# Optimization experiments

Hardware: AMD Instinct MI355X
Metric: run time of the kernel (lower is better)

## Reference

```python
import jax, jax.numpy as jnp
import numpy as np
from jax import lax

# Module config (from init_kwargs)
PADDING = (1, 1)
DILATION = (1, 1)
GROUPS = 1
# stride param is initialized to ones(2); effective integer stride = floor(stride) = (1, 1).
# Output shape depends on this value, so it must be static under jit.
INT_STRIDE = (1, 1)


def setup_inputs() -> dict:
    key = jax.random.key(0)
    k1, k2 = jax.random.split(key)
    B, Cin, H, W = 32, 128, 64, 64
    Cout, kH, kW = 256, 3, 3
    x = jax.random.normal(k1, (B, Cin, H, W), dtype=jnp.float32)
    # reset_parameters: uniform(-stdv, stdv), stdv = 1/sqrt(Cin*kH*kW)
    stdv = 1.0 / np.sqrt(Cin * kH * kW)
    weight = jax.random.uniform(k2, (Cout, Cin // GROUPS, kH, kW), dtype=jnp.float32,
                                minval=-stdv, maxval=stdv)
    stride = jnp.ones((2,), dtype=jnp.float32)
    return {"x": x, "weight": weight, "stride": stride}


def reference(x, weight, stride):
    # Integer strides = floor(stride); with stride initialized to ones this is (1, 1).
    # (Static under jit; floor has zero derivative a.e., so stride only affects
    #  sampling locations, exactly as in the CUDA im2col forward.)
    out = lax.conv_general_dilated(
        x, weight,
        window_strides=INT_STRIDE,
        padding=[(PADDING[0], PADDING[0]), (PADDING[1], PADDING[1])],
        rhs_dilation=DILATION,
        dimension_numbers=("NCHW", "OIHW", "NCHW"),
        feature_group_count=GROUPS,
    )
    return out
```

## Files before the change

### kernel.cpp

```cpp
#include <hip/hip_runtime.h>

typedef __attribute__((ext_vector_type(8))) short short8;
typedef __attribute__((ext_vector_type(4))) float f32x4;

#define XP_ELEMS (32u * 66u * 66u * 128u)
#define WT_ELEMS (256u * 1152u)
#define WS_NEED  ((size_t)(XP_ELEMS + WT_ELEMS) * 2u)

typedef const __attribute__((address_space(1))) void* gp1_t;
typedef __attribute__((address_space(3))) void* lp3_t;

__device__ __forceinline__ void gload16(const void* g, void* l) {
  __builtin_amdgcn_global_load_lds((gp1_t)g, (lp3_t)l, 16, 0, 0);
}

__device__ __forceinline__ short f2bf(float f) {
  unsigned u = __float_as_uint(f);
  u = (u + 0x7FFFu + ((u >> 16) & 1u)) >> 16;
  return (short)u;
}

__global__ __launch_bounds__(256) void prepass_x(const float* __restrict__ x,
                                                 short* __restrict__ xp) {
  __shared__ short lds[64 * 128];
  const int y = blockIdx.x;
  const int b = blockIdx.y;
  const int t = threadIdx.x;

  const float* src = x + (long)b * 128 * 4096 + y * 64;
#pragma unroll
  for (int i = 0; i < 8; ++i) {
    int f4 = t + i * 256;
    int cin = f4 >> 4, px4 = f4 & 15;
    float4 v = *(const float4*)(src + (long)cin * 4096 + px4 * 4);
    float vv[4] = {v.x, v.y, v.z, v.w};
#pragma unroll
    for (int j = 0; j < 4; ++j) {
      int px = px4 * 4 + j;
      int g = (cin >> 3) ^ ((px ^ (px >> 2)) & 15);
      lds[px * 128 + (g << 3) + (cin & 7)] = f2bf(vv[j]);
    }
  }
  __syncthreads();
  short* dst = xp + ((long)(b * 66 + y + 1) * 66 + 1) * 128;
#pragma unroll
  for (int i = 0; i < 4; ++i) {
    int f8 = t + i * 256;
    int px = f8 >> 4, c8 = f8 & 15;
    int g = c8 ^ ((px ^ (px >> 2)) & 15);
    short8 v = *(const short8*)&lds[px * 128 + (g << 3)];
    *(short8*)(dst + (long)px * 128 + c8 * 8) = v;
  }
  short8 z = (short8)0;
  short* rowbase = xp + (long)(b * 66 + y + 1) * 66 * 128;
  if (t < 32) {
    int px = (t < 16) ? 0 : 65;
    int c8 = t & 15;
    *(short8*)(rowbase + (long)px * 128 + c8 * 8) = z;
  }
  if (y == 0) {
    short* r0 = xp + (long)(b * 66) * 66 * 128;
    for (int idx = t; idx < 66 * 16; idx += 256) *(short8*)(r0 + idx * 8) = z;
  }
  if (y == 63) {
    short* r65 = xp + ((long)(b * 66) + 65) * 66 * 128;
    for (int idx = t; idx < 66 * 16; idx += 256) *(short8*)(r65 + idx * 8) = z;
  }
}

__global__ __launch_bounds__(256) void prepass_w(const float* __restrict__ w,
                                                 short* __restrict__ wt) {
  int o    = blockIdx.x * 256 + threadIdx.x;
  int cout = o / 1152;
  int r    = o % 1152;
  int kh   = r / 384;
  int kw   = (r / 128) % 3;
  int cin  = r & 127;
  wt[o] = f2bf(w[((cout * 128 + cin) * 3 + kh) * 3 + kw]);
}

__global__ __launch_bounds__(256) void conv_gemm(const short* __restrict__ xp,
                                                 const short* __restrict__ wt,
                                                 float* __restrict__ out) {
  __shared__ short Alds[2 * 128 * 32];
  __shared__ short Blds[2 * 128 * 32];
  const int tid   = threadIdx.x;
  const int w     = tid >> 6;
  const int l     = tid & 63;
  const int l15   = l & 15;
  const int q     = l >> 4;
  const int ntile = blockIdx.x;
  const int m0    = blockIdx.y << 7;

  const int srow = (w << 4) + (l >> 2);
  const int sch8 = (((l & 3) ^ ((srow >> 1) & 3)) * 8);

  const long aoff0 = (long)(m0 + srow) * 1152 + sch8;
  const long aoff1 = aoff0 + (long)64 * 1152;

  long boff[2];
#pragma unroll
  for (int c = 0; c < 2; ++c) {
    int ng = (ntile << 7) + (c << 6) + srow;
    int b = ng >> 12, yx = ng & 4095;
    int y = yx >> 6, xx = yx & 63;
    boff[c] = ((long)(b * 66 + y) * 66 + xx) * 128 + sch8;
  }

  short* Adst0 = &Alds[(w << 4) * 32];
  short* Adst1 = Adst0 + 64 * 32;
  short* Bdst0 = &Blds[(w << 4) * 32];
  short* Bdst1 = Bdst0 + 64 * 32;

  f32x4 acc[4][4];
#pragma unroll
  for (int i = 0; i < 4; ++i)
#pragma unroll
    for (int j = 0; j < 4; ++j) acc[i][j] = (f32x4)0.f;

  const int wm = (w >> 1) << 6;
  const int wn = (w & 1) << 6;

#pragma unroll
  for (int khkw = 0; khkw < 9; ++khkw) {
    const int kh = khkw / 3, kw = khkw % 3;
    const long sB = (long)(kh * 66 + kw) * 128;
    const int kkb = khkw << 7;
#pragma unroll
    for (int s = 0; s < 2; ++s) {
#pragma unroll
      for (int c = 0; c < 2; ++c) {
        const int cin0 = (s << 6) + (c << 5);
        const int kk0  = kkb + cin0;
        const int co   = c * 4096;
        gload16(wt + aoff0 + kk0, Adst0 + co);
        gload16(wt + aoff1 + kk0, Adst1 + co);
        gload16(xp + boff[0] + sB + cin0, Bdst0 + co);
        gload16(xp + boff[1] + sB + cin0, Bdst1 + co);
      }
      __syncthreads();
#pragma unroll
      for (int c = 0; c < 2; ++c) {
        const int co = c * 4096;
        short8 af[4], bf[4];
#pragma unroll
        for (int i = 0; i < 4; ++i) {
          int rA = wm + (i << 4) + l15;
          af[i] = *(const short8*)&Alds[co + rA * 32 + ((q ^ ((rA >> 1) & 3)) << 3)];
        }
#pragma unroll
        for (int j = 0; j < 4; ++j) {
          int rB = wn + (j << 4) + l15;
          bf[j] = *(const short8*)&Blds[co + rB * 32 + ((q ^ ((rB >> 1) & 3)) << 3)];
        }
#pragma unroll
        for (int i = 0; i < 4; ++i)
#pragma unroll
          for (int j = 0; j < 4; ++j)
            acc[i][j] = __builtin_amdgcn_mfma_f32_16x16x32_bf16(af[i], bf[j],
                                                                acc[i][j], 0, 0, 0);
      }
      __syncthreads();
    }
  }

  const int ngb = (ntile << 7) + wn;
  const int b   = ngb >> 12;
  const int yxb = ngb & 4095;
  float* outb = out + (long)b * (256 * 4096) + yxb + l15;
#pragma unroll
  for (int i = 0; i < 4; ++i) {
#pragma unroll
    for (int r = 0; r < 4; ++r) {
      const int cout = m0 + wm + (i << 4) + q * 4 + r;
      float* orow = outb + (long)cout * 4096;
#pragma unroll
      for (int j = 0; j < 4; ++j) orow[j * 16] = acc[i][j][r];
    }
  }
}

__global__ __launch_bounds__(256) void naive_conv(const float* __restrict__ x,
                                                  const float* __restrict__ wgt,
                                                  float* __restrict__ out) {
  long o = (long)blockIdx.x * 256 + threadIdx.x;
  int xx = (int)(o & 63);
  int y  = (int)((o >> 6) & 63);
  int co = (int)((o >> 12) & 255);
  int b  = (int)(o >> 20);
  float s = 0.f;
  for (int ci = 0; ci < 128; ++ci) {
    for (int kh = 0; kh < 3; ++kh) {
      int iy = y + kh - 1;
      if (iy < 0 || iy > 63) continue;
      for (int kw = 0; kw < 3; ++kw) {
        int ix = xx + kw - 1;
        if (ix < 0 || ix > 63) continue;
        s += x[((long)(b * 128 + ci) * 64 + iy) * 64 + ix] *
             wgt[((co * 128 + ci) * 3 + kh) * 3 + kw];
      }
    }
  }
  out[o] = s;
}

extern "C" void kernel_launch(void* const* d_in, const int* in_sizes, int n_in,
                              void* d_out, int out_size, void* d_ws, size_t ws_size,
                              hipStream_t stream) {
  (void)in_sizes; (void)n_in;
  const float* x   = (const float*)d_in[0];
  const float* wgt = (const float*)d_in[1];
  float* out = (float*)d_out;
  if (ws_size >= WS_NEED) {
    short* xp = (short*)d_ws;
    short* wt = xp + XP_ELEMS;
    prepass_x<<<dim3(64, 32), dim3(256), 0, stream>>>(x, xp);
    prepass_w<<<dim3(WT_ELEMS / 256), dim3(256), 0, stream>>>(wgt, wt);
    conv_gemm<<<dim3(1024, 2), dim3(256), 0, stream>>>(xp, wt, out);
  } else {
    naive_conv<<<dim3(out_size / 256), dim3(256), 0, stream>>>(x, wgt, out);
  }
}
```

Measured before the change: 264.2 us.

## Enlarge GEMM tile to 256x256 with a 4-stage async LDS pipeline

The implicit-GEMM conv kernel now computes a full 256-cout by 256-pixel tile per 512-thread block, so each block covers all output channels and the input tile is read once instead of twice. A 4-deep ring of LDS buffers is filled with global_load_lds three stages ahead, and explicit vmcnt waits replace the two full barriers per k-step that the old version used. MFMA sections are bracketed with raised wave priority. Each wave now holds 32 accumulators, which raises register pressure, and the grid drops to 512 blocks, which may affect occupancy and load balance across CUs.

Result: faster. 258.3 us (-2.2%).

```diff
diff --git a/kernel.cpp b/kernel.cpp
--- a/kernel.cpp
+++ b/kernel.cpp
@@ -79,103 +79,115 @@
   wt[o] = f2bf(w[((cout * 128 + cin) * 3 + kh) * 3 + kw]);
 }
 
-__global__ __launch_bounds__(256) void conv_gemm(const short* __restrict__ xp,
-                                                 const short* __restrict__ wt,
-                                                 float* __restrict__ out) {
-  __shared__ short Alds[2 * 128 * 32];
-  __shared__ short Blds[2 * 128 * 32];
-  const int tid   = threadIdx.x;
-  const int w     = tid >> 6;
-  const int l     = tid & 63;
-  const int l15   = l & 15;
-  const int q     = l >> 4;
+__global__ __launch_bounds__(512, 2) void conv_gemm(const short* __restrict__ xp,
+                                                    const short* __restrict__ wt,
+                                                    float* __restrict__ out) {
+  __shared__ alignas(16) short Al[4][256 * 32];
+  __shared__ alignas(16) short Bl[4][256 * 32];
+  const int tid = threadIdx.x;
+  const int w   = tid >> 6;
+  const int l   = tid & 63;
+  const int l15 = l & 15;
+  const int q   = l >> 4;
+  const int wm2 = w >> 2;
+  const int wn4 = w & 3;
   const int ntile = blockIdx.x;
-  const int m0    = blockIdx.y << 7;
-
-  const int srow = (w << 4) + (l >> 2);
-  const int sch8 = (((l & 3) ^ ((srow >> 1) & 3)) * 8);
-
-  const long aoff0 = (long)(m0 + srow) * 1152 + sch8;
-  const long aoff1 = aoff0 + (long)64 * 1152;
-
-  long boff[2];
-#pragma unroll
-  for (int c = 0; c < 2; ++c) {
-    int ng = (ntile << 7) + (c << 6) + srow;
-    int b = ng >> 12, yx = ng & 4095;
-    int y = yx >> 6, xx = yx & 63;
-    boff[c] = ((long)(b * 66 + y) * 66 + xx) * 128 + sch8;
-  }
-
-  short* Adst0 = &Alds[(w << 4) * 32];
-  short* Adst1 = Adst0 + 64 * 32;
-  short* Bdst0 = &Blds[(w << 4) * 32];
-  short* Bdst1 = Bdst0 + 64 * 32;
-
-  f32x4 acc[4][4];
-#pragma unroll
-  for (int i = 0; i < 4; ++i)
-#pragma unroll
-    for (int j = 0; j < 4; ++j) acc[i][j] = (f32x4)0.f;
-
-  const int wm = (w >> 1) << 6;
-  const int wn = (w & 1) << 6;
-
-#pragma unroll
-  for (int khkw = 0; khkw < 9; ++khkw) {
-    const int kh = khkw / 3, kw = khkw % 3;
-    const long sB = (long)(kh * 66 + kw) * 128;
-    const int kkb = khkw << 7;
-#pragma unroll
-    for (int s = 0; s < 2; ++s) {
-#pragma unroll
-      for (int c = 0; c < 2; ++c) {
-        const int cin0 = (s << 6) + (c << 5);
-        const int kk0  = kkb + cin0;
-        const int co   = c * 4096;
-        gload16(wt + aoff0 + kk0, Adst0 + co);
-        gload16(wt + aoff1 + kk0, Adst1 + co);
-        gload16(xp + boff[0] + sB + cin0, Bdst0 + co);
-        gload16(xp + boff[1] + sB + cin0, Bdst1 + co);
-      }
-      __syncthreads();
-#pragma unroll
-      for (int c = 0; c < 2; ++c) {
-        const int co = c * 4096;
-        short8 af[4], bf[4];
-#pragma unroll
-        for (int i = 0; i < 4; ++i) {
-          int rA = wm + (i << 4) + l15;
-          af[i] = *(const short8*)&Alds[co + rA * 32 + ((q ^ ((rA >> 1) & 3)) << 3)];
-        }
-#pragma unroll
-        for (int j = 0; j < 4; ++j) {
-          int rB = wn + (j << 4) + l15;
-          bf[j] = *(const short8*)&Blds[co + rB * 32 + ((q ^ ((rB >> 1) & 3)) << 3)];
-        }
-#pragma unroll
-        for (int i = 0; i < 4; ++i)
-#pragma unroll
-          for (int j = 0; j < 4; ++j)
-            acc[i][j] = __builtin_amdgcn_mfma_f32_16x16x32_bf16(af[i], bf[j],
-                                                                acc[i][j], 0, 0, 0);
-      }
-      __syncthreads();
-    }
-  }
-
-  const int ngb = (ntile << 7) + wn;
-  const int b   = ngb >> 12;
-  const int yxb = ngb & 4095;
-  float* outb = out + (long)b * (256 * 4096) + yxb + l15;
-#pragma unroll
-  for (int i = 0; i < 4; ++i) {
+
+  const int r0  = tid >> 2;
+  const int r1  = r0 + 128;
+  const int p0  = tid & 3;
+  const int cs0 = p0 ^ ((r0 >> 1) & 3);
+  const int cs1 = p0 ^ ((r1 >> 1) & 3);
+  const long aoff0 = (long)r0 * 1152 + (cs0 << 3);
+  const long aoff1 = (long)r1 * 1152 + (cs1 << 3);
+
+  long boff0, boff1;
+  {
+    int n0 = (ntile << 8) + r0;
+    int bb = n0 >> 12, yx = n0 & 4095, y = yx >> 6, xx = yx & 63;
+    boff0 = ((long)(bb * 66 + y) * 66 + xx) * 128 + (cs0 << 3);
+    int n1 = n0 + 128;
+    bb = n1 >> 12; yx = n1 & 4095; y = yx >> 6; xx = yx & 63;
+    boff1 = ((long)(bb * 66 + y) * 66 + xx) * 128 + (cs1 << 3);
+  }
+  const int ldst0 = tid * 8;
+  const int ldst1 = (512 + tid) * 8;
+
+  int aRd[8], bRd[4];
+#pragma unroll
+  for (int mi = 0; mi < 8; ++mi) {
+    int r = (wm2 << 7) + (mi << 4) + l15;
+    aRd[mi] = r * 32 + ((q ^ ((r >> 1) & 3)) << 3);
+  }
+#pragma unroll
+  for (int nj = 0; nj < 4; ++nj) {
+    int r = (wn4 << 6) + (nj << 4) + l15;
+    bRd[nj] = r * 32 + ((q ^ ((r >> 1) & 3)) << 3);
+  }
+
+  f32x4 acc[8][4];
+#pragma unroll
+  for (int mi = 0; mi < 8; ++mi)
+#pragma unroll
+    for (int nj = 0; nj < 4; ++nj) acc[mi][nj] = (f32x4)0.f;
+
+  auto STAGE = [&](int kss, int bufS) {
+    const int kq = kss >> 2;
+    const int kh = kq / 3, kw2 = kq % 3;
+    const long sBs = (long)(kh * 66 + kw2) * 128 + ((kss & 3) << 5);
+    const long ka  = (long)kss << 5;
+    gload16(wt + aoff0 + ka, &Al[bufS][ldst0]);
+    gload16(wt + aoff1 + ka, &Al[bufS][ldst1]);
+    gload16(xp + boff0 + sBs, &Bl[bufS][ldst0]);
+    gload16(xp + boff1 + sBs, &Bl[bufS][ldst1]);
+  };
+
+  STAGE(0, 0); STAGE(1, 1); STAGE(2, 2);
+  asm volatile("s_waitcnt vmcnt(8)" ::: "memory");
+  __builtin_amdgcn_s_barrier();
+  __builtin_amdgcn_sched_barrier(0);
+
+#pragma unroll
+  for (int ks = 0; ks < 36; ++ks) {
+    if (ks + 3 < 36) STAGE(ks + 3, (ks + 3) & 3);
+
+    const short* Ab = &Al[ks & 3][0];
+    const short* Bb = &Bl[ks & 3][0];
+    short8 af[8], bf[4];
+#pragma unroll
+    for (int mi = 0; mi < 8; ++mi) af[mi] = *(const short8*)&Ab[aRd[mi]];
+#pragma unroll
+    for (int nj = 0; nj < 4; ++nj) bf[nj] = *(const short8*)&Bb[bRd[nj]];
+
+    __builtin_amdgcn_s_setprio(1);
+#pragma unroll
+    for (int mi = 0; mi < 8; ++mi)
+#pragma unroll
+      for (int nj = 0; nj < 4; ++nj)
+        acc[mi][nj] = __builtin_amdgcn_mfma_f32_16x16x32_bf16(af[mi], bf[nj],
+                                                              acc[mi][nj], 0, 0, 0);
+    __builtin_amdgcn_s_setprio(0);
+
+    if (ks + 1 < 36) {
+      if (ks + 3 < 36)      asm volatile("s_waitcnt vmcnt(8)" ::: "memory");
+      else if (ks + 2 < 36) asm volatile("s_waitcnt vmcnt(4)" ::: "memory");
+      else                  asm volatile("s_waitcnt vmcnt(0)" ::: "memory");
+      __builtin_amdgcn_s_barrier();
+      __builtin_amdgcn_sched_barrier(0);
+    }
+  }
+
+  const int bimg = ntile >> 4;
+  const int yx0  = ((ntile & 15) << 8) + (wn4 << 6) + l15;
+  float* outb = out + (long)bimg * (256 * 4096) + yx0;
+#pragma unroll
+  for (int mi = 0; mi < 8; ++mi) {
 #pragma unroll
     for (int r = 0; r < 4; ++r) {
-      const int cout = m0 + wm + (i << 4) + q * 4 + r;
+      const int cout = (wm2 << 7) + (mi << 4) + (q << 2) + r;
       float* orow = outb + (long)cout * 4096;
 #pragma unroll
-      for (int j = 0; j < 4; ++j) orow[j * 16] = acc[i][j][r];
+      for (int nj = 0; nj < 4; ++nj) orow[nj << 4] = acc[mi][nj][r];
     }
   }
 }
@@ -216,7 +228,7 @@
     short* wt = xp + XP_ELEMS;
     prepass_x<<<dim3(64, 32), dim3(256), 0, stream>>>(x, xp);
     prepass_w<<<dim3(WT_ELEMS / 256), dim3(256), 0, stream>>>(wgt, wt);
-    conv_gemm<<<dim3(1024, 2), dim3(256), 0, stream>>>(xp, wt, out);
+    conv_gemm<<<dim3(512), dim3(512), 0, stream>>>(xp, wt, out);
   } else {
     naive_conv<<<dim3(out_size / 256), dim3(256), 0, stream>>>(x, wgt, out);
   }
```

## Triple-buffer conv GEMM K-loop with async LDS prefetch and one barrier per step

Applied to the files above, without the earlier changes.

Replaces the synchronous two-barrier-per-chunk K loop with a 3-slot ring buffer. Global-to-LDS loads for step k+2 are issued before computing step k, and each step waits only on vmcnt plus a single barrier. It also precomputes LDS read offsets, raises MFMA wave priority with s_setprio, and adds a launch-bounds occupancy hint of 3. The cost is 50% more LDS per block and a reliance on hand-counted vmcnt waits being correct for the buffered loads.

Measured after the change: 277.6 us. +5.1%, slower.

```diff
diff --git a/kernel.cpp b/kernel.cpp
--- a/kernel.cpp
+++ b/kernel.cpp
@@ -79,11 +79,11 @@
   wt[o] = f2bf(w[((cout * 128 + cin) * 3 + kh) * 3 + kw]);
 }
 
-__global__ __launch_bounds__(256) void conv_gemm(const short* __restrict__ xp,
-                                                 const short* __restrict__ wt,
-                                                 float* __restrict__ out) {
-  __shared__ short Alds[2 * 128 * 32];
-  __shared__ short Blds[2 * 128 * 32];
+__global__ __launch_bounds__(256, 3) void conv_gemm(const short* __restrict__ xp,
+                                                    const short* __restrict__ wt,
+                                                    float* __restrict__ out) {
+  __shared__ alignas(16) short Alds[3 * 128 * 32];
+  __shared__ alignas(16) short Blds[3 * 128 * 32];
   const int tid   = threadIdx.x;
   const int w     = tid >> 6;
   const int l     = tid & 63;
@@ -92,77 +92,92 @@
   const int ntile = blockIdx.x;
   const int m0    = blockIdx.y << 7;
 
-  const int srow = (w << 4) + (l >> 2);
-  const int sch8 = (((l & 3) ^ ((srow >> 1) & 3)) * 8);
-
-  const long aoff0 = (long)(m0 + srow) * 1152 + sch8;
+  const int r  = tid >> 2;
+  const int p  = tid & 3;
+  const int cs = p ^ ((r >> 1) & 3);
+  const long aoff0 = (long)(m0 + r) * 1152 + (cs << 3);
   const long aoff1 = aoff0 + (long)64 * 1152;
-
-  long boff[2];
-#pragma unroll
-  for (int c = 0; c < 2; ++c) {
-    int ng = (ntile << 7) + (c << 6) + srow;
-    int b = ng >> 12, yx = ng & 4095;
-    int y = yx >> 6, xx = yx & 63;
-    boff[c] = ((long)(b * 66 + y) * 66 + xx) * 128 + sch8;
-  }
-
-  short* Adst0 = &Alds[(w << 4) * 32];
-  short* Adst1 = Adst0 + 64 * 32;
-  short* Bdst0 = &Blds[(w << 4) * 32];
-  short* Bdst1 = Bdst0 + 64 * 32;
-
-  f32x4 acc[4][4];
-#pragma unroll
-  for (int i = 0; i < 4; ++i)
-#pragma unroll
-    for (int j = 0; j < 4; ++j) acc[i][j] = (f32x4)0.f;
+  long boff0, boff1;
+  {
+    int n0 = (ntile << 7) + r;
+    int bb = n0 >> 12, yy = (n0 >> 6) & 63, xx = n0 & 63;
+    boff0 = ((long)(bb * 66 + yy) * 66 + xx) * 128 + (cs << 3);
+    int n1 = n0 + 64;
+    bb = n1 >> 12; yy = (n1 >> 6) & 63; xx = n1 & 63;
+    boff1 = ((long)(bb * 66 + yy) * 66 + xx) * 128 + (cs << 3);
+  }
+  const int ldst0 = r * 32 + p * 8;
+  const int ldst1 = ldst0 + 2048;
 
   const int wm = (w >> 1) << 6;
   const int wn = (w & 1) << 6;
-
-#pragma unroll
-  for (int khkw = 0; khkw < 9; ++khkw) {
-    const int kh = khkw / 3, kw = khkw % 3;
-    const long sB = (long)(kh * 66 + kw) * 128;
-    const int kkb = khkw << 7;
-#pragma unroll
-    for (int s = 0; s < 2; ++s) {
-#pragma unroll
-      for (int c = 0; c < 2; ++c) {
-        const int cin0 = (s << 6) + (c << 5);
-        const int kk0  = kkb + cin0;
-        const int co   = c * 4096;
-        gload16(wt + aoff0 + kk0, Adst0 + co);
-        gload16(wt + aoff1 + kk0, Adst1 + co);
-        gload16(xp + boff[0] + sB + cin0, Bdst0 + co);
-        gload16(xp + boff[1] + sB + cin0, Bdst1 + co);
-      }
-      __syncthreads();
-#pragma unroll
-      for (int c = 0; c < 2; ++c) {
-        const int co = c * 4096;
-        short8 af[4], bf[4];
-#pragma unroll
-        for (int i = 0; i < 4; ++i) {
-          int rA = wm + (i << 4) + l15;
-          af[i] = *(const short8*)&Alds[co + rA * 32 + ((q ^ ((rA >> 1) & 3)) << 3)];
-        }
-#pragma unroll
-        for (int j = 0; j < 4; ++j) {
-          int rB = wn + (j << 4) + l15;
-          bf[j] = *(const short8*)&Blds[co + rB * 32 + ((q ^ ((rB >> 1) & 3)) << 3)];
-        }
-#pragma unroll
-        for (int i = 0; i < 4; ++i)
-#pragma unroll
-          for (int j = 0; j < 4; ++j)
-            acc[i][j] = __builtin_amdgcn_mfma_f32_16x16x32_bf16(af[i], bf[j],
-                                                                acc[i][j], 0, 0, 0);
-      }
-      __syncthreads();
-    }
-  }
+  int aRd[4], bRd[4];
+#pragma unroll
+  for (int i = 0; i < 4; ++i) {
+    int rA = wm + (i << 4) + l15;
+    aRd[i] = rA * 32 + ((q ^ ((rA >> 1) & 3)) << 3);
+    int rB = wn + (i << 4) + l15;
+    bRd[i] = rB * 32 + ((q ^ ((rB >> 1) & 3)) << 3);
+  }
+
+  f32x4 acc[4][4];
+#pragma unroll
+  for (int i = 0; i < 4; ++i)
+#pragma unroll
+    for (int j = 0; j < 4; ++j) acc[i][j] = (f32x4)0.f;
+
+  auto STAGE = [&](int slot, int ks) {
+    const int kq  = ks >> 2;
+    const int kh  = kq / 3, kw2 = kq - kh * 3;
+    const int sB  = (kh * 66 + kw2) * 128 + ((ks & 3) << 5);
+    const int ka  = ks << 5;
+    short* Ad = &Alds[slot * 4096];
+    short* Bd = &Blds[slot * 4096];
+    gload16(wt + aoff0 + ka, Ad + ldst0);
+    gload16(wt + aoff1 + ka, Ad + ldst1);
+    gload16(xp + boff0 + sB, Bd + ldst0);
+    gload16(xp + boff1 + sB, Bd + ldst1);
+  };
+
+  auto COMPUTE = [&](int slot) {
+    const short* Ab = &Alds[slot * 4096];
+    const short* Bb = &Blds[slot * 4096];
+    short8 af[4], bf[4];
+#pragma unroll
+    for (int i = 0; i < 4; ++i) af[i] = *(const short8*)&Ab[aRd[i]];
+#pragma unroll
+    for (int j = 0; j < 4; ++j) bf[j] = *(const short8*)&Bb[bRd[j]];
+    __builtin_amdgcn_s_setprio(1);
+#pragma unroll
+    for (int i = 0; i < 4; ++i)
+#pragma unroll
+      for (int j = 0; j < 4; ++j)
+        acc[i][j] = __builtin_amdgcn_mfma_f32_16x16x32_bf16(af[i], bf[j],
+                                                            acc[i][j], 0, 0, 0);
+    __builtin_amdgcn_s_setprio(0);
+  };
+
+#define BAR()   __builtin_amdgcn_s_barrier()
+#define VMC(n)  asm volatile("s_waitcnt vmcnt(" #n ")" ::: "memory")
+
+  STAGE(0, 0);
+  STAGE(1, 1);
+  VMC(4);
+  BAR();
+
+  int s_cur = 0, s_nxt = 1, s_stg = 2;
+#pragma unroll 1
+  for (int ks = 0; ks < 34; ++ks) {
+    STAGE(s_stg, ks + 2);
+    COMPUTE(s_cur);
+    VMC(4);
+    BAR();
+    int t0 = s_cur; s_cur = s_nxt; s_nxt = s_stg; s_stg = t0;
+  }
+  COMPUTE(s_cur);
+  VMC(0);
+  BAR();
+  COMPUTE(s_nxt);
 
   const int ngb = (ntile << 7) + wn;
   const int b   = ngb >> 12;
@@ -171,13 +186,15 @@
 #pragma unroll
   for (int i = 0; i < 4; ++i) {
 #pragma unroll
-    for (int r = 0; r < 4; ++r) {
-      const int cout = m0 + wm + (i << 4) + q * 4 + r;
+    for (int rr = 0; rr < 4; ++rr) {
+      const int cout = m0 + wm + (i << 4) + q * 4 + rr;
       float* orow = outb + (long)cout * 4096;
 #pragma unroll
-      for (int j = 0; j < 4; ++j) orow[j * 16] = acc[i][j][r];
+      for (int j = 0; j < 4; ++j) orow[j * 16] = acc[i][j][rr];
     }
   }
+#undef BAR
+#undef VMC
 }
 
 __global__ __launch_bounds__(256) void naive_conv(const float* __restrict__ x,
```
